# Performance work log

Hardware: AMD Instinct MI355X
Metric: run time of the kernel (lower is better)

Reference implementation:

```python
import jax, jax.numpy as jnp
import numpy as np

FP8_MAX = 448.0  # float8_e4m3fn max representable magnitude


def _to_fp8(x):
    # round-to-nearest fp8_e4m3 simulation via dtype cast
    return jnp.clip(x, -FP8_MAX, FP8_MAX).astype(jnp.float8_e4m3fn).astype(jnp.float32)


def setup_inputs() -> dict:
    key = jax.random.key(0)
    ks = jax.random.split(key, 8)
    T, H, I, E, K = 4096, 2048, 4096, 8, 2

    x = jax.random.normal(ks[0], (T, H), dtype=jnp.float32)
    selected_experts = jax.random.randint(ks[1], (T, K), 0, E, dtype=jnp.int32)
    rw = jax.random.uniform(ks[2], (T, K), dtype=jnp.float32) + 1e-3
    routing_weights = rw / jnp.sum(rw, axis=-1, keepdims=True)

    # float master weights -> per-tensor fp8 quantized buffers + weight scales
    w1_f = jax.random.normal(ks[3], (E, 2 * I, H), dtype=jnp.float32) * 0.02
    w2_f = jax.random.normal(ks[4], (E, H, I), dtype=jnp.float32) * 0.02
    w1_wscale = jnp.max(jnp.abs(w1_f), axis=(1, 2)) / FP8_MAX  # [E]
    w2_wscale = jnp.max(jnp.abs(w2_f), axis=(1, 2)) / FP8_MAX
    w1 = _to_fp8(w1_f / w1_wscale[:, None, None])  # fp8 values stored as f32
    w2 = _to_fp8(w2_f / w2_wscale[:, None, None])

    # per-tensor activation input scales (amax-style calibration constants)
    w1_iscale = jnp.full((E,), 4.0 / FP8_MAX, dtype=jnp.float32)
    w2_iscale = jnp.full((E,), 8.0 / FP8_MAX, dtype=jnp.float32)

    return {
        "x": x,
        "selected_experts": selected_experts,
        "routing_weights": routing_weights,
        "w1": w1,
        "w2": w2,
        "w1_iscale": w1_iscale,
        "w2_iscale": w2_iscale,
        "w1_wscale": w1_wscale,
        "w2_wscale": w2_wscale,
    }


def _fp8_linear(x, w_fp8, iscale, wscale):
    xq = _to_fp8(x / iscale)  # [T, in]
    return (xq @ w_fp8.T) * (iscale * wscale)  # [T, out]


def reference(x, selected_experts, routing_weights, w1, w2,
              w1_iscale, w2_iscale, w1_wscale, w2_wscale):
    E = w1.shape[0]
    I = w2.shape[2]
    out = jnp.zeros_like(x)
    for e in range(E):  # fixed small expert loop
        # combined routing weight for this expert per token: [T]
        gate = jnp.sum(
            jnp.where(selected_experts == e, routing_weights, 0.0), axis=-1)
        h = _fp8_linear(x, w1[e], w1_iscale[e], w1_wscale[e])  # [T, 2I]
        g, u = h[:, :I], h[:, I:]
        a = jax.nn.silu(g) * u  # gated activation
        y = _fp8_linear(a, w2[e], w2_iscale[e], w2_wscale[e])  # [T, H]
        out = out + gate[:, None] * y
    return out
```

## Files before the change

kernel.cpp:

```cpp
#include <hip/hip_runtime.h>
#include <cstdint>
#include <cstddef>

#define T_TOK 4096
#define H_DIM 2048
#define I_DIM 4096
#define E_NUM 8
#define CAP_ROWS 9216

#define OFF_COUNTS   0
#define OFF_CURSOR   64
#define OFF_PADOFF   128
#define OFF_TOKIDX   1024
#define OFF_TOKGATE  (OFF_TOKIDX + CAP_ROWS*4)
#define OFF_XQ       ((size_t)(OFF_TOKGATE + CAP_ROWS*4))
#define XQ_BYTES     ((size_t)CAP_ROWS*H_DIM)
#define OFF_AQ       (OFF_XQ + XQ_BYTES)
#define AQ_BYTES     ((size_t)CAP_ROWS*I_DIM)
#define OFF_W1B      (OFF_AQ + AQ_BYTES)
#define W1B_BYTES    ((size_t)E_NUM*2*I_DIM*H_DIM)
#define OFF_W2B      (OFF_W1B + W1B_BYTES)

typedef float f32x4 __attribute__((ext_vector_type(4)));

__device__ __forceinline__ float fp8_round(float v) {
  v = fminf(448.f, fmaxf(-448.f, v));
  float av = fabsf(v);
  if (av < 0.015625f) {
    return rintf(v * 512.f) * (1.f / 512.f);
  }
  unsigned u = __float_as_uint(v);
  unsigned lsb = (u >> 20) & 1u;
  u += 0x7FFFFu + lsb;
  u &= 0xFFF00000u;
  return __uint_as_float(u);
}

__device__ __forceinline__ unsigned fp8_enc(float q) {
  unsigned u = __float_as_uint(q);
  unsigned s = (u >> 24) & 0x80u;
  float aq = fabsf(q);
  if (aq < 0.015625f) {
    return s | (unsigned)(int)rintf(aq * 512.f);
  }
  unsigned e = (u >> 23) & 0xFFu;
  unsigned man = (u >> 20) & 7u;
  return s | ((e - 120u) << 3) | man;
}

__device__ __forceinline__ void gld16(const void* g, void* l) {
  __builtin_amdgcn_global_load_lds(
      (__attribute__((address_space(1))) void*)((void*)g),
      (__attribute__((address_space(3))) void*)l, 16, 0, 0);
}

__global__ void k_count(const int* __restrict__ se, int* __restrict__ counts) {
  int t = blockIdx.x * 256 + threadIdx.x;
  if (t >= T_TOK) return;
  int e0 = se[t * 2], e1 = se[t * 2 + 1];
  atomicAdd(&counts[e0], 1);
  if (e1 != e0) atomicAdd(&counts[e1], 1);
}

__global__ void k_offsets(const int* __restrict__ counts, int* __restrict__ padOff) {
  if (threadIdx.x == 0 && blockIdx.x == 0) {
    int acc = 0;
    for (int e = 0; e < E_NUM; e++) {
      padOff[e] = acc;
      acc += ((counts[e] + 127) / 128) * 128;
    }
    padOff[E_NUM] = acc;
  }
}

__global__ void k_fill(const int* __restrict__ se, const float* __restrict__ rw,
                       const int* __restrict__ padOff, int* __restrict__ cursor,
                       int* __restrict__ tokIdx, float* __restrict__ tokGate) {
  int t = blockIdx.x * 256 + threadIdx.x;
  if (t >= T_TOK) return;
  int e0 = se[t * 2], e1 = se[t * 2 + 1];
  float w0 = rw[t * 2], w1 = rw[t * 2 + 1];
  float g0 = w0 + (e1 == e0 ? w1 : 0.f);
  int s0 = atomicAdd(&cursor[e0], 1);
  tokIdx[padOff[e0] + s0] = t;
  tokGate[padOff[e0] + s0] = g0;
  if (e1 != e0) {
    int s1 = atomicAdd(&cursor[e1], 1);
    tokIdx[padOff[e1] + s1] = t;
    tokGate[padOff[e1] + s1] = w1;
  }
}

__global__ __launch_bounds__(256)
void k_gather(const float* __restrict__ x, const int* __restrict__ padOff,
              const int* __restrict__ counts, const int* __restrict__ tokIdx,
              const float* __restrict__ w1_is, unsigned char* __restrict__ xq) {
  const int rblk = blockIdx.x;
  const int total = padOff[E_NUM];
  if (rblk >= total) return;
  int e = 0;
  while (rblk >= padOff[e + 1]) e++;
  unsigned char* dst = xq + (size_t)rblk * H_DIM;
  const int c = threadIdx.x * 8;
  const int local = rblk - padOff[e];
  if (local >= counts[e]) {
    *(uint2*)(dst + c) = make_uint2(0u, 0u);
    return;
  }
  const int tok = tokIdx[rblk];
  const float is = w1_is[e];
  const float* src = x + (size_t)tok * H_DIM + c;
  float4 v0 = *(const float4*)(src);
  float4 v1 = *(const float4*)(src + 4);
  unsigned lo = fp8_enc(fp8_round(v0.x / is))
              | (fp8_enc(fp8_round(v0.y / is)) << 8)
              | (fp8_enc(fp8_round(v0.z / is)) << 16)
              | (fp8_enc(fp8_round(v0.w / is)) << 24);
  unsigned hi = fp8_enc(fp8_round(v1.x / is))
              | (fp8_enc(fp8_round(v1.y / is)) << 8)
              | (fp8_enc(fp8_round(v1.z / is)) << 16)
              | (fp8_enc(fp8_round(v1.w / is)) << 24);
  *(uint2*)(dst + c) = make_uint2(lo, hi);
}

__global__ __launch_bounds__(256)
void k_wconv(const float* __restrict__ w, unsigned char* __restrict__ o, long n8) {
  long i = (long)blockIdx.x * 256 + threadIdx.x;
  if (i >= n8) return;
  const float4* src = (const float4*)w + i * 2;
  float4 v0 = src[0];
  float4 v1 = src[1];
  unsigned lo = fp8_enc(v0.x) | (fp8_enc(v0.y) << 8) | (fp8_enc(v0.z) << 16) | (fp8_enc(v0.w) << 24);
  unsigned hi = fp8_enc(v1.x) | (fp8_enc(v1.y) << 8) | (fp8_enc(v1.z) << 16) | (fp8_enc(v1.w) << 24);
  ((uint2*)o)[i] = make_uint2(lo, hi);
}

__global__ __launch_bounds__(512, 1)
void k_gemm1(const unsigned char* __restrict__ xq,
             const unsigned char* __restrict__ w1b,
             const int* __restrict__ padOff,
             const float* __restrict__ w1_is, const float* __restrict__ w1_ws,
             const float* __restrict__ w2_is,
             unsigned char* __restrict__ aq) {
  const int e = blockIdx.z;
  const int rbase = padOff[e];
  const int rows = padOff[e + 1] - rbase;
  const int mt = blockIdx.y;
  if (mt * 128 >= rows) return;
  const int nt = blockIdx.x;

  __shared__ __align__(16) unsigned char As[128 * 64];
  __shared__ __align__(16) unsigned char Bg[128 * 64];
  __shared__ __align__(16) unsigned char Bu[128 * 64];

  const int tid = threadIdx.x;
  const int lane = tid & 63;
  const int wave = tid >> 6;
  const int wm = wave >> 2, wn = wave & 3;
  const int lr = lane & 15, quad = lane >> 4;
  const int qh = quad >> 1, ql = quad & 1;
  const int swz = (lr >> 2) & 3;
  const int cs0 = (((0 + qh) ^ swz) << 4) + ql * 8;
  const int cs1 = (((2 + qh) ^ swz) << 4) + ql * 8;

  const int r = tid >> 2;
  const int kb = tid & 3;
  const int kbs = (kb ^ ((r >> 2) & 3)) * 16;
  const unsigned char* pa = xq + (size_t)(rbase + mt * 128 + r) * H_DIM + kbs;
  const unsigned char* pg = w1b + ((size_t)e * 2 * I_DIM + nt * 128 + r) * H_DIM + kbs;
  const unsigned char* pu = pg + (size_t)I_DIM * H_DIM;
  unsigned char* la = As + tid * 16;
  unsigned char* lg = Bg + tid * 16;
  unsigned char* lu = Bu + tid * 16;

  f32x4 accg[4][2] = {};
  f32x4 accu[4][2] = {};

  for (int k0 = 0; k0 < H_DIM; k0 += 64) {
    gld16(pa + k0, la);
    gld16(pg + k0, lg);
    gld16(pu + k0, lu);
    __syncthreads();
    long af[4][2], gf[2][2], uf[2][2];
#pragma unroll
    for (int i = 0; i < 4; i++) {
      const unsigned char* ba = As + (wm * 64 + i * 16 + lr) * 64;
      af[i][0] = *(const long*)(ba + cs0);
      af[i][1] = *(const long*)(ba + cs1);
    }
#pragma unroll
    for (int j = 0; j < 2; j++) {
      const unsigned char* bg = Bg + (wn * 32 + j * 16 + lr) * 64;
      const unsigned char* bu = Bu + (wn * 32 + j * 16 + lr) * 64;
      gf[j][0] = *(const long*)(bg + cs0);
      gf[j][1] = *(const long*)(bg + cs1);
      uf[j][0] = *(const long*)(bu + cs0);
      uf[j][1] = *(const long*)(bu + cs1);
    }
#pragma unroll
    for (int i = 0; i < 4; i++)
#pragma unroll
      for (int j = 0; j < 2; j++) {
        accg[i][j] = __builtin_amdgcn_mfma_f32_16x16x32_fp8_fp8(af[i][0], gf[j][0], accg[i][j], 0, 0, 0);
        accg[i][j] = __builtin_amdgcn_mfma_f32_16x16x32_fp8_fp8(af[i][1], gf[j][1], accg[i][j], 0, 0, 0);
        accu[i][j] = __builtin_amdgcn_mfma_f32_16x16x32_fp8_fp8(af[i][0], uf[j][0], accu[i][j], 0, 0, 0);
        accu[i][j] = __builtin_amdgcn_mfma_f32_16x16x32_fp8_fp8(af[i][1], uf[j][1], accu[i][j], 0, 0, 0);
      }
    __syncthreads();
  }

  const float s1 = w1_is[e] * w1_ws[e];
  const float is2 = w2_is[e];
#pragma unroll
  for (int i = 0; i < 4; i++)
#pragma unroll
    for (int j = 0; j < 2; j++)
#pragma unroll
      for (int rr = 0; rr < 4; rr++) {
        const int row = wm * 64 + i * 16 + quad * 4 + rr;
        const int col = nt * 128 + wn * 32 + j * 16 + lr;
        float g = accg[i][j][rr] * s1;
        float u = accu[i][j][rr] * s1;
        float a = (g / (1.f + expf(-g))) * u;
        float q = fp8_round(a / is2);
        aq[(size_t)(rbase + mt * 128 + row) * I_DIM + col] = (unsigned char)fp8_enc(q);
      }
}

__global__ __launch_bounds__(512, 1)
void k_gemm2(const unsigned char* __restrict__ aq,
             const unsigned char* __restrict__ w2b,
             const int* __restrict__ padOff, const int* __restrict__ counts,
             const int* __restrict__ tokIdx, const float* __restrict__ tokGate,
             const float* __restrict__ w2_is, const float* __restrict__ w2_ws,
             float* __restrict__ out) {
  const int e = blockIdx.z;
  const int rbase = padOff[e];
  const int rows = padOff[e + 1] - rbase;
  const int mt = blockIdx.y;
  if (mt * 128 >= rows) return;
  const int nt = blockIdx.x;
  const int cnt = counts[e];

  __shared__ __align__(16) unsigned char As[128 * 64];
  __shared__ __align__(16) unsigned char Bs[128 * 64];
  __shared__ int sTok[128];
  __shared__ float sGate[128];

  const int tid = threadIdx.x;
  const int lane = tid & 63;
  const int wave = tid >> 6;
  const int wm = wave >> 2, wn = wave & 3;
  const int lr = lane & 15, quad = lane >> 4;
  const int qh = quad >> 1, ql = quad & 1;
  const int swz = (lr >> 2) & 3;
  const int cs0 = (((0 + qh) ^ swz) << 4) + ql * 8;
  const int cs1 = (((2 + qh) ^ swz) << 4) + ql * 8;

  if (tid < 128) {
    int rr = mt * 128 + tid;
    if (rr < cnt) { sTok[tid] = tokIdx[rbase + rr]; sGate[tid] = tokGate[rbase + rr]; }
    else          { sTok[tid] = -1;                 sGate[tid] = 0.f; }
  }

  const int r = tid >> 2;
  const int kb = tid & 3;
  const int kbs = (kb ^ ((r >> 2) & 3)) * 16;
  const unsigned char* pa = aq + (size_t)(rbase + mt * 128 + r) * I_DIM + kbs;
  const unsigned char* pb = w2b + ((size_t)e * H_DIM + nt * 128 + r) * I_DIM + kbs;
  unsigned char* la = As + tid * 16;
  unsigned char* lb = Bs + tid * 16;

  f32x4 acc[4][2] = {};

  for (int k0 = 0; k0 < I_DIM; k0 += 64) {
    gld16(pa + k0, la);
    gld16(pb + k0, lb);
    __syncthreads();
    long af[4][2], bf[2][2];
#pragma unroll
    for (int i = 0; i < 4; i++) {
      const unsigned char* ba = As + (wm * 64 + i * 16 + lr) * 64;
      af[i][0] = *(const long*)(ba + cs0);
      af[i][1] = *(const long*)(ba + cs1);
    }
#pragma unroll
    for (int j = 0; j < 2; j++) {
      const unsigned char* bb = Bs + (wn * 32 + j * 16 + lr) * 64;
      bf[j][0] = *(const long*)(bb + cs0);
      bf[j][1] = *(const long*)(bb + cs1);
    }
#pragma unroll
    for (int i = 0; i < 4; i++)
#pragma unroll
      for (int j = 0; j < 2; j++) {
        acc[i][j] = __builtin_amdgcn_mfma_f32_16x16x32_fp8_fp8(af[i][0], bf[j][0], acc[i][j], 0, 0, 0);
        acc[i][j] = __builtin_amdgcn_mfma_f32_16x16x32_fp8_fp8(af[i][1], bf[j][1], acc[i][j], 0, 0, 0);
      }
    __syncthreads();
  }

  const float s2 = w2_is[e] * w2_ws[e];
#pragma unroll
  for (int i = 0; i < 4; i++)
#pragma unroll
    for (int j = 0; j < 2; j++)
#pragma unroll
      for (int rr = 0; rr < 4; rr++) {
        const int row = wm * 64 + i * 16 + quad * 4 + rr;
        const int tk = sTok[row];
        if (tk >= 0) {
          const int col = nt * 128 + wn * 32 + j * 16 + lr;
          unsafeAtomicAdd(out + (size_t)tk * H_DIM + col, sGate[row] * s2 * acc[i][j][rr]);
        }
      }
}

extern "C" void kernel_launch(void* const* d_in, const int* in_sizes, int n_in,
                              void* d_out, int out_size, void* d_ws, size_t ws_size,
                              hipStream_t stream) {
  const float* x     = (const float*)d_in[0];
  const int*   se    = (const int*)d_in[1];
  const float* rw    = (const float*)d_in[2];
  const float* w1    = (const float*)d_in[3];
  const float* w2    = (const float*)d_in[4];
  const float* w1_is = (const float*)d_in[5];
  const float* w2_is = (const float*)d_in[6];
  const float* w1_ws = (const float*)d_in[7];
  const float* w2_ws = (const float*)d_in[8];
  float* out = (float*)d_out;
  char* ws = (char*)d_ws;

  int*   counts  = (int*)(ws + OFF_COUNTS);
  int*   cursor  = (int*)(ws + OFF_CURSOR);
  int*   padOff  = (int*)(ws + OFF_PADOFF);
  int*   tokIdx  = (int*)(ws + OFF_TOKIDX);
  float* tokGate = (float*)(ws + OFF_TOKGATE);
  unsigned char* xq  = (unsigned char*)(ws + OFF_XQ);
  unsigned char* aq  = (unsigned char*)(ws + OFF_AQ);
  unsigned char* w1b = (unsigned char*)(ws + OFF_W1B);
  unsigned char* w2b = (unsigned char*)(ws + OFF_W2B);

  hipMemsetAsync(ws, 0, 1024, stream);
  hipMemsetAsync(d_out, 0, (size_t)T_TOK * H_DIM * sizeof(float), stream);

  k_count  <<<16, 256, 0, stream>>>(se, counts);
  k_offsets<<<1, 1, 0, stream>>>(counts, padOff);
  k_fill   <<<16, 256, 0, stream>>>(se, rw, padOff, cursor, tokIdx, tokGate);
  k_gather <<<CAP_ROWS, 256, 0, stream>>>(x, padOff, counts, tokIdx, w1_is, xq);

  k_wconv<<<65536, 256, 0, stream>>>(w1, w1b, (long)E_NUM * 2 * I_DIM * H_DIM / 8);
  k_wconv<<<32768, 256, 0, stream>>>(w2, w2b, (long)E_NUM * H_DIM * I_DIM / 8);

  dim3 g1(I_DIM / 128, 32, E_NUM);
  k_gemm1<<<g1, 512, 0, stream>>>(xq, w1b, padOff, w1_is, w1_ws, w2_is, aq);

  dim3 g2(H_DIM / 128, 32, E_NUM);
  k_gemm2<<<g2, 512, 0, stream>>>(aq, w2b, padOff, counts, tokIdx, tokGate, w2_is, w2_ws, out);
}
```

Baseline: 1.386 ms.

## Switch FP8 GEMMs to 16x16x128 scaled MFMA with K=128 tiles

Both expert GEMMs now use the MI355X scaled f8f6f4 MFMA (16x16x128) with a unit block scale in place of pairs of 16x16x32 fp8 MFMAs. The K tile per iteration grows from 64 to 128 bytes, with a new 8-way XOR swizzle for the LDS layout and 128-bit LDS fragment reads. This cuts MFMA issue count, LDS read instructions and barrier/loop overhead per unit of work. In exchange it doubles LDS use, and correctness depends on the operand lane layout matching the new swizzle and the unit scale encoding.

```diff
diff --git a/kernel.cpp b/kernel.cpp
--- a/kernel.cpp
+++ b/kernel.cpp
@@ -22,6 +22,10 @@
 #define OFF_W2B      (OFF_W1B + W1B_BYTES)
 
 typedef float f32x4 __attribute__((ext_vector_type(4)));
+typedef int   i32x4 __attribute__((ext_vector_type(4)));
+typedef int   i32x8 __attribute__((ext_vector_type(8)));
+
+#define UNIT_SCALE 0x7F7F7F7Fu
 
 __device__ __forceinline__ float fp8_round(float v) {
   v = fminf(448.f, fmaxf(-448.f, v));
@@ -52,6 +56,12 @@
   __builtin_amdgcn_global_load_lds(
       (__attribute__((address_space(1))) void*)((void*)g),
       (__attribute__((address_space(3))) void*)l, 16, 0, 0);
+}
+
+__device__ __forceinline__ i32x8 rd32(const unsigned char* row, int cs0, int cs1) {
+  i32x4 lo = *(const i32x4*)(row + cs0);
+  i32x4 hi = *(const i32x4*)(row + cs1);
+  return __builtin_shufflevector(lo, hi, 0, 1, 2, 3, 4, 5, 6, 7);
 }
 
 __global__ void k_count(const int* __restrict__ se, int* __restrict__ counts) {
@@ -149,63 +159,56 @@
   if (mt * 128 >= rows) return;
   const int nt = blockIdx.x;
 
-  __shared__ __align__(16) unsigned char As[128 * 64];
-  __shared__ __align__(16) unsigned char Bg[128 * 64];
-  __shared__ __align__(16) unsigned char Bu[128 * 64];
+  __shared__ __align__(16) unsigned char As[128 * 128];
+  __shared__ __align__(16) unsigned char Bg[128 * 128];
+  __shared__ __align__(16) unsigned char Bu[128 * 128];
 
   const int tid = threadIdx.x;
   const int lane = tid & 63;
   const int wave = tid >> 6;
   const int wm = wave >> 2, wn = wave & 3;
   const int lr = lane & 15, quad = lane >> 4;
-  const int qh = quad >> 1, ql = quad & 1;
-  const int swz = (lr >> 2) & 3;
-  const int cs0 = (((0 + qh) ^ swz) << 4) + ql * 8;
-  const int cs1 = (((2 + qh) ^ swz) << 4) + ql * 8;
-
-  const int r = tid >> 2;
-  const int kb = tid & 3;
-  const int kbs = (kb ^ ((r >> 2) & 3)) * 16;
-  const unsigned char* pa = xq + (size_t)(rbase + mt * 128 + r) * H_DIM + kbs;
-  const unsigned char* pg = w1b + ((size_t)e * 2 * I_DIM + nt * 128 + r) * H_DIM + kbs;
-  const unsigned char* pu = pg + (size_t)I_DIM * H_DIM;
-  unsigned char* la = As + tid * 16;
-  unsigned char* lg = Bg + tid * 16;
-  unsigned char* lu = Bu + tid * 16;
+  const int swz = lr & 7;
+  const int cs0 = (((2 * quad)     ^ swz) << 4);
+  const int cs1 = (((2 * quad + 1) ^ swz) << 4);
+
+  const int sr0 = tid >> 3;
+  const int scol = ((tid & 7) ^ (sr0 & 7)) << 4;
+  const unsigned char* paL = xq + (size_t)(rbase + mt * 128 + sr0) * H_DIM + scol;
+  const unsigned char* paH = paL + (size_t)64 * H_DIM;
+  const unsigned char* pgL = w1b + ((size_t)e * 2 * I_DIM + nt * 128 + sr0) * H_DIM + scol;
+  const unsigned char* pgH = pgL + (size_t)64 * H_DIM;
+  const unsigned char* puL = pgL + (size_t)I_DIM * H_DIM;
+  const unsigned char* puH = pgH + (size_t)I_DIM * H_DIM;
+  unsigned char* laL = As + tid * 16; unsigned char* laH = laL + 8192;
+  unsigned char* lgL = Bg + tid * 16; unsigned char* lgH = lgL + 8192;
+  unsigned char* luL = Bu + tid * 16; unsigned char* luH = luL + 8192;
 
   f32x4 accg[4][2] = {};
   f32x4 accu[4][2] = {};
 
-  for (int k0 = 0; k0 < H_DIM; k0 += 64) {
-    gld16(pa + k0, la);
-    gld16(pg + k0, lg);
-    gld16(pu + k0, lu);
+  for (int k0 = 0; k0 < H_DIM; k0 += 128) {
+    gld16(paL + k0, laL); gld16(paH + k0, laH);
+    gld16(pgL + k0, lgL); gld16(pgH + k0, lgH);
+    gld16(puL + k0, luL); gld16(puH + k0, luH);
     __syncthreads();
-    long af[4][2], gf[2][2], uf[2][2];
+    i32x8 gf[2], uf[2];
+#pragma unroll
+    for (int j = 0; j < 2; j++) {
+      gf[j] = rd32(Bg + (wn * 32 + j * 16 + lr) * 128, cs0, cs1);
+      uf[j] = rd32(Bu + (wn * 32 + j * 16 + lr) * 128, cs0, cs1);
+    }
 #pragma unroll
     for (int i = 0; i < 4; i++) {
-      const unsigned char* ba = As + (wm * 64 + i * 16 + lr) * 64;
-      af[i][0] = *(const long*)(ba + cs0);
-      af[i][1] = *(const long*)(ba + cs1);
+      i32x8 a = rd32(As + (wm * 64 + i * 16 + lr) * 128, cs0, cs1);
+#pragma unroll
+      for (int j = 0; j < 2; j++) {
+        accg[i][j] = __builtin_amdgcn_mfma_scale_f32_16x16x128_f8f6f4(
+            a, gf[j], accg[i][j], 0, 0, 0, UNIT_SCALE, 0, UNIT_SCALE);
+        accu[i][j] = __builtin_amdgcn_mfma_scale_f32_16x16x128_f8f6f4(
+            a, uf[j], accu[i][j], 0, 0, 0, UNIT_SCALE, 0, UNIT_SCALE);
+      }
     }
-#pragma unroll
-    for (int j = 0; j < 2; j++) {
-      const unsigned char* bg = Bg + (wn * 32 + j * 16 + lr) * 64;
-      const unsigned char* bu = Bu + (wn * 32 + j * 16 + lr) * 64;
-      gf[j][0] = *(const long*)(bg + cs0);
-      gf[j][1] = *(const long*)(bg + cs1);
-      uf[j][0] = *(const long*)(bu + cs0);
-      uf[j][1] = *(const long*)(bu + cs1);
-    }
-#pragma unroll
-    for (int i = 0; i < 4; i++)
-#pragma unroll
-      for (int j = 0; j < 2; j++) {
-        accg[i][j] = __builtin_amdgcn_mfma_f32_16x16x32_fp8_fp8(af[i][0], gf[j][0], accg[i][j], 0, 0, 0);
-        accg[i][j] = __builtin_amdgcn_mfma_f32_16x16x32_fp8_fp8(af[i][1], gf[j][1], accg[i][j], 0, 0, 0);
-        accu[i][j] = __builtin_amdgcn_mfma_f32_16x16x32_fp8_fp8(af[i][0], uf[j][0], accu[i][j], 0, 0, 0);
-        accu[i][j] = __builtin_amdgcn_mfma_f32_16x16x32_fp8_fp8(af[i][1], uf[j][1], accu[i][j], 0, 0, 0);
-      }
     __syncthreads();
   }
 
@@ -242,8 +245,8 @@
   const int nt = blockIdx.x;
   const int cnt = counts[e];
 
-  __shared__ __align__(16) unsigned char As[128 * 64];
-  __shared__ __align__(16) unsigned char Bs[128 * 64];
+  __shared__ __align__(16) unsigned char As[128 * 128];
+  __shared__ __align__(16) unsigned char Bs[128 * 128];
   __shared__ int sTok[128];
   __shared__ float sGate[128];
 
@@ -252,10 +255,9 @@
   const int wave = tid >> 6;
   const int wm = wave >> 2, wn = wave & 3;
   const int lr = lane & 15, quad = lane >> 4;
-  const int qh = quad >> 1, ql = quad & 1;
-  const int swz = (lr >> 2) & 3;
-  const int cs0 = (((0 + qh) ^ swz) << 4) + ql * 8;
-  const int cs1 = (((2 + qh) ^ swz) << 4) + ql * 8;
+  const int swz = lr & 7;
+  const int cs0 = (((2 * quad)     ^ swz) << 4);
+  const int cs1 = (((2 * quad + 1) ^ swz) << 4);
 
   if (tid < 128) {
     int rr = mt * 128 + tid;
@@ -263,40 +265,33 @@
     else          { sTok[tid] = -1;                 sGate[tid] = 0.f; }
   }
 
-  const int r = tid >> 2;
-  const int kb = tid & 3;
-  const int kbs = (kb ^ ((r >> 2) & 3)) * 16;
-  const unsigned char* pa = aq + (size_t)(rbase + mt * 128 + r) * I_DIM + kbs;
-  const unsigned char* pb = w2b + ((size_t)e * H_DIM + nt * 128 + r) * I_DIM + kbs;
-  unsigned char* la = As + tid * 16;
-  unsigned char* lb = Bs + tid * 16;
+  const int sr0 = tid >> 3;
+  const int scol = ((tid & 7) ^ (sr0 & 7)) << 4;
+  const unsigned char* paL = aq + (size_t)(rbase + mt * 128 + sr0) * I_DIM + scol;
+  const unsigned char* paH = paL + (size_t)64 * I_DIM;
+  const unsigned char* pbL = w2b + ((size_t)e * H_DIM + nt * 128 + sr0) * I_DIM + scol;
+  const unsigned char* pbH = pbL + (size_t)64 * I_DIM;
+  unsigned char* laL = As + tid * 16; unsigned char* laH = laL + 8192;
+  unsigned char* lbL = Bs + tid * 16; unsigned char* lbH = lbL + 8192;
 
   f32x4 acc[4][2] = {};
 
-  for (int k0 = 0; k0 < I_DIM; k0 += 64) {
-    gld16(pa + k0, la);
-    gld16(pb + k0, lb);
+  for (int k0 = 0; k0 < I_DIM; k0 += 128) {
+    gld16(paL + k0, laL); gld16(paH + k0, laH);
+    gld16(pbL + k0, lbL); gld16(pbH + k0, lbH);
     __syncthreads();
-    long af[4][2], bf[2][2];
+    i32x8 bf[2];
+#pragma unroll
+    for (int j = 0; j < 2; j++)
+      bf[j] = rd32(Bs + (wn * 32 + j * 16 + lr) * 128, cs0, cs1);
 #pragma unroll
     for (int i = 0; i < 4; i++) {
-      const unsigned char* ba = As + (wm * 64 + i * 16 + lr) * 64;
-      af[i][0] = *(const long*)(ba + cs0);
-      af[i][1] = *(const long*)(ba + cs1);
+      i32x8 a = rd32(As + (wm * 64 + i * 16 + lr) * 128, cs0, cs1);
+#pragma unroll
+      for (int j = 0; j < 2; j++)
+        acc[i][j] = __builtin_amdgcn_mfma_scale_f32_16x16x128_f8f6f4(
+            a, bf[j], acc[i][j], 0, 0, 0, UNIT_SCALE, 0, UNIT_SCALE);
     }
-#pragma unroll
-    for (int j = 0; j < 2; j++) {
-      const unsigned char* bb = Bs + (wn * 32 + j * 16 + lr) * 64;
-      bf[j][0] = *(const long*)(bb + cs0);
-      bf[j][1] = *(const long*)(bb + cs1);
-    }
-#pragma unroll
-    for (int i = 0; i < 4; i++)
-#pragma unroll
-      for (int j = 0; j < 2; j++) {
-        acc[i][j] = __builtin_amdgcn_mfma_f32_16x16x32_fp8_fp8(af[i][0], bf[j][0], acc[i][j], 0, 0, 0);
-        acc[i][j] = __builtin_amdgcn_mfma_f32_16x16x32_fp8_fp8(af[i][1], bf[j][1], acc[i][j], 0, 0, 0);
-      }
     __syncthreads();
   }
 
```

New measurement: 4.758 ms. 243% more time.
